# Kernel optimization log

Measured on AMD Instinct MI355X. Metric: run time of the kernel, lower is better.

## Reference

```python
import jax, jax.numpy as jnp
import numpy as np

B, T, N, E = 16, 24, 300, 9600
H, F = 3, 8            # num_heads, out_feats of EdgeGAT
GRU_H = 16
NUM_AIRPORTS, HORIZON = 300, 24
NEG_SLOPE = 0.2


def setup_inputs() -> dict:
    key = jax.random.key(0)
    ks = jax.random.split(key, 16)
    s = 0.1
    x = jax.random.normal(ks[0], (B, T, N, 1), jnp.float32)
    edge_weight = jax.random.uniform(ks[1], (B, T, E, 1), jnp.float32)
    src = jax.random.randint(ks[2], (E,), 0, N)
    dst = jax.random.randint(ks[3], (E,), 0, N)
    W_node = jax.random.normal(ks[4], (1, H * F), jnp.float32) * s
    W_edge = jax.random.normal(ks[5], (1, H * F), jnp.float32) * s
    attn_l = jax.random.normal(ks[6], (H, F), jnp.float32) * s
    attn_r = jax.random.normal(ks[7], (H, F), jnp.float32) * s
    attn_e = jax.random.normal(ks[8], (H, F), jnp.float32) * s
    gat_bias = jax.random.normal(ks[9], (H * F,), jnp.float32) * s
    W_ih = jax.random.normal(ks[10], (3 * GRU_H, H * F), jnp.float32) * s
    W_hh = jax.random.normal(ks[11], (3 * GRU_H, GRU_H), jnp.float32) * s
    b_ih = jax.random.normal(ks[12], (3 * GRU_H,), jnp.float32) * s
    b_hh = jax.random.normal(ks[13], (3 * GRU_H,), jnp.float32) * s
    W_fc = jax.random.normal(ks[14], (NUM_AIRPORTS * HORIZON, GRU_H), jnp.float32) * s
    b_fc = jax.random.normal(ks[15], (NUM_AIRPORTS * HORIZON,), jnp.float32) * s
    return dict(x=x, edge_weight=edge_weight, W_node=W_node, W_edge=W_edge,
                attn_l=attn_l, attn_r=attn_r, attn_e=attn_e, gat_bias=gat_bias,
                W_ih=W_ih, W_hh=W_hh, b_ih=b_ih, b_hh=b_hh,
                W_fc=W_fc, b_fc=b_fc, src=src, dst=dst)


def _forward(x, edge_weight, W_node, W_edge, attn_l, attn_r, attn_e, gat_bias,
             W_ih, W_hh, b_ih, b_hh, W_fc, b_fc, src, dst):
    # --- EdgeGAT on all B*T graphs at once (shared topology, varying feats) ---
    feat = (x @ W_node).reshape(B, T, N, H, F)            # [B,T,N,H,F]
    fe = (edge_weight @ W_edge).reshape(B, T, E, H, F)    # [B,T,E,H,F]
    el = jnp.einsum('btnhf,hf->btnh', feat, attn_l)       # [B,T,N,H]
    er = jnp.einsum('btnhf,hf->btnh', feat, attn_r)
    ee = jnp.einsum('btehf,hf->bteh', fe, attn_e)
    e = jax.nn.leaky_relu(el[:, :, src] + er[:, :, dst] + ee, NEG_SLOPE)  # [B,T,E,H]
    # edge softmax over incoming edges of each dst node
    e_t = jnp.moveaxis(e, 2, 0)                           # [E,B,T,H]
    m = jax.ops.segment_max(e_t, dst, num_segments=N)     # [N,B,T,H]
    num = jnp.exp(e_t - m[dst])
    den = jax.ops.segment_sum(num, dst, num_segments=N)
    alpha = num / den[dst]                                # [E,B,T,H]
    ft_src = jnp.moveaxis(feat[:, :, src], 2, 0)          # [E,B,T,H,F]
    rst = jax.ops.segment_sum(ft_src * alpha[..., None], dst, num_segments=N)  # [N,B,T,H,F]
    rst = rst.reshape(N, B, T, H * F) + gat_bias          # bias of EdgeGATConv
    # mean-pool over nodes per graph -> GRU input sequence
    gru_in = rst.mean(axis=0)                             # [B,T,24]
    # --- GRU (torch semantics), return final hidden state ---
    def step(h, xt):
        gi = xt @ W_ih.T + b_ih
        gh = h @ W_hh.T + b_hh
        i_r, i_z, i_n = jnp.split(gi, 3, axis=-1)
        h_r, h_z, h_n = jnp.split(gh, 3, axis=-1)
        r = jax.nn.sigmoid(i_r + h_r)
        z = jax.nn.sigmoid(i_z + h_z)
        n = jnp.tanh(i_n + r * h_n)
        return (1.0 - z) * n + z * h, None
    h0 = jnp.zeros((B, GRU_H), gru_in.dtype)
    h_n, _ = jax.lax.scan(step, h0, jnp.moveaxis(gru_in, 1, 0))  # scan over T
    return h_n @ W_fc.T + b_fc                            # [B, num_airports*horizon]


def reference(x, edge_weight, W_node, W_edge, attn_l, attn_r, attn_e, gat_bias,
              W_ih, W_hh, b_ih, b_hh, W_fc, b_fc, src, dst):
    return _forward(x, edge_weight, W_node, W_edge, attn_l, attn_r, attn_e, gat_bias,
                    W_ih, W_hh, b_ih, b_hh, W_fc, b_fc, src, dst)
```

## Files before the change

kernel.cpp:

```cpp
#include <hip/hip_runtime.h>
#include <math.h>

#define B_ 16
#define T_ 24
#define G_ 384
#define N_ 300
#define E_ 9600
#define H_ 3
#define F_ 8
#define HF_ 24
#define GRUH_ 16
#define OUTB_ 7200
#define TPB_ 640
#define NWC_ 10

__global__ __launch_bounds__(TPB_) void gat_kernel(
    const float* __restrict__ x, const float* __restrict__ ew,
    const float* __restrict__ Wn, const float* __restrict__ We,
    const float* __restrict__ al, const float* __restrict__ ar,
    const float* __restrict__ ae,
    const int* __restrict__ src, const int* __restrict__ dst,
    float* __restrict__ S)
{
    __shared__ unsigned pkl[E_];
    __shared__ int cnt[NWC_ * N_];
    __shared__ int tot[N_];
    __shared__ int rps[N_ + 1];
    __shared__ float xs[N_];
    __shared__ float cf[9];
    __shared__ float Sred[NWC_][3];

    const int g = blockIdx.x;
    const int tid = threadIdx.x;
    const int w = tid >> 6;
    const long base_e = (long)g * E_;

    for (int i = tid; i < N_; i += TPB_) xs[i] = x[g * N_ + i];
    if (tid < H_) {
        int h = tid;
        float cl = 0.f, cr = 0.f, ce = 0.f;
        #pragma unroll
        for (int f = 0; f < F_; ++f) {
            float wn = Wn[h * F_ + f];
            cl += wn * al[h * F_ + f];
            cr += wn * ar[h * F_ + f];
            ce += We[h * F_ + f] * ae[h * F_ + f];
        }
        cf[h] = cl; cf[3 + h] = cr; cf[6 + h] = ce;
    }

    for (int i = tid; i < NWC_ * N_; i += TPB_) cnt[i] = 0;
    __syncthreads();
    for (int i = tid; i < E_; i += TPB_) atomicAdd(&cnt[w * N_ + dst[i]], 1);
    __syncthreads();
    if (tid < N_) {
        int run = 0;
        #pragma unroll
        for (int k = 0; k < NWC_; ++k) {
            int t = cnt[k * N_ + tid];
            cnt[k * N_ + tid] = run;
            run += t;
        }
        tot[tid] = run;
    }
    __syncthreads();
    if (tid < 64) {
        int base = 0;
        for (int c = 0; c < 5; ++c) {
            int i = c * 64 + tid;
            int orig = (i < N_) ? tot[i] : 0;
            int v = orig;
            #pragma unroll
            for (int o = 1; o < 64; o <<= 1) {
                int u = __shfl_up(v, o, 64);
                if (tid >= o) v += u;
            }
            if (i < N_) rps[i] = base + v - orig;
            base += __shfl(v, 63, 64);
        }
        if (tid == 0) rps[N_] = base;
    }
    __syncthreads();
    for (int i = tid; i < E_; i += TPB_) {
        int d = dst[i];
        int pos = rps[d] + atomicAdd(&cnt[w * N_ + d], 1);
        pkl[pos] = (unsigned)i | ((unsigned)src[i] << 17);
    }
    __syncthreads();

    float n0 = 0.f, d0 = 0.f, n1 = 0.f, d1 = 0.f, n2 = 0.f, d2 = 0.f;
    if (tid < 2 * N_) {
        const int n = tid >> 1;
        const int half = tid & 1;
        const float xd = xs[n];
        const float c0l = cf[0], c1l = cf[1], c2l = cf[2];
        const float c0r = cf[3], c1r = cf[4], c2r = cf[5];
        const float c0e = cf[6], c1e = cf[7], c2e = cf[8];
        const int p1 = rps[n + 1];
        for (int p = rps[n] + half; p < p1; p += 2) {
            unsigned pkv = pkl[p];
            float wv = ew[base_e + (pkv & 0x1FFFFu)];
            float xsv = xs[pkv >> 17];
            float e0 = fmaf(xsv, c0l, fmaf(xd, c0r, wv * c0e)); e0 = e0 > 0.f ? e0 : 0.2f * e0;
            float e1 = fmaf(xsv, c1l, fmaf(xd, c1r, wv * c1e)); e1 = e1 > 0.f ? e1 : 0.2f * e1;
            float e2 = fmaf(xsv, c2l, fmaf(xd, c2r, wv * c2e)); e2 = e2 > 0.f ? e2 : 0.2f * e2;
            float p0 = __expf(e0), pe1 = __expf(e1), pe2 = __expf(e2);
            d0 += p0;  n0 += p0 * xsv;
            d1 += pe1; n1 += pe1 * xsv;
            d2 += pe2; n2 += pe2 * xsv;
        }
    }
    n0 += __shfl_xor(n0, 1); d0 += __shfl_xor(d0, 1);
    n1 += __shfl_xor(n1, 1); d1 += __shfl_xor(d1, 1);
    n2 += __shfl_xor(n2, 1); d2 += __shfl_xor(d2, 1);
    float a0 = 0.f, a1 = 0.f, a2 = 0.f;
    if (tid < 2 * N_ && (tid & 1) == 0) {
        a0 = d0 > 0.f ? n0 / d0 : 0.f;
        a1 = d1 > 0.f ? n1 / d1 : 0.f;
        a2 = d2 > 0.f ? n2 / d2 : 0.f;
    }
    for (int o = 32; o; o >>= 1) {
        a0 += __shfl_down(a0, o);
        a1 += __shfl_down(a1, o);
        a2 += __shfl_down(a2, o);
    }
    const int wave = tid >> 6, lane = tid & 63;
    if (lane == 0) { Sred[wave][0] = a0; Sred[wave][1] = a1; Sred[wave][2] = a2; }
    __syncthreads();
    if (tid < 3) {
        float s = 0.f;
        #pragma unroll
        for (int w2 = 0; w2 < NWC_; ++w2) s += Sred[w2][tid];
        S[g * 3 + tid] = s;
    }
}

__global__ __launch_bounds__(256) void fc_kernel(
    const float* __restrict__ S, const float* __restrict__ Wn,
    const float* __restrict__ gb, const float* __restrict__ Wih,
    const float* __restrict__ bih, const float* __restrict__ Whh,
    const float* __restrict__ bhh, const float* __restrict__ Wfc,
    const float* __restrict__ bfc, float* __restrict__ out)
{
    __shared__ float S2[2][T_][H_];
    __shared__ float hS[2][GRUH_];
    const int tid = threadIdx.x;
    const int idx0 = blockIdx.x * 256;
    const int b0 = idx0 / OUTB_;

    if (tid < 2 * T_ * H_) {
        const int grp = tid / (T_ * H_);
        const int rem = tid - grp * (T_ * H_);
        const int t = rem / H_, h = rem - t * H_;
        const int bb = b0 + grp;
        float s = 0.f;
        if (bb < B_) s = S[(bb * T_ + t) * H_ + h];
        S2[grp][t][h] = s * (1.0f / N_);
    }
    __syncthreads();

    if (tid < 64) {
        const int grp = tid >> 4;
        const int u = tid & 15;
        const int gbase = tid & ~15;
        const bool active = (grp < 2) && (b0 + grp < B_);
        const int sgrp = active ? grp : 0;

        float whr[GRUH_], whz[GRUH_], whn[GRUH_];
        #pragma unroll
        for (int k = 0; k < GRUH_; ++k) {
            whr[k] = Whh[u * GRUH_ + k];
            whz[k] = Whh[(16 + u) * GRUH_ + k];
            whn[k] = Whh[(32 + u) * GRUH_ + k];
        }
        const float bhr = bhh[u], bhz = bhh[16 + u], bhn = bhh[32 + u];

        float A[3][3], C[3];
        #pragma unroll
        for (int r = 0; r < 3; ++r) {
            const int j = r * 16 + u;
            float cc = bih[j];
            A[r][0] = A[r][1] = A[r][2] = 0.f;
            #pragma unroll
            for (int k = 0; k < HF_; ++k) {
                float wk = Wih[j * HF_ + k];
                cc += wk * gb[k];
                A[r][k >> 3] += wk * Wn[k];
            }
            C[r] = cc;
        }

        float h = 0.f;
        for (int t = 0; t < T_; ++t) {
            float S0 = S2[sgrp][t][0], S1 = S2[sgrp][t][1], Sv2 = S2[sgrp][t][2];
            float gr = C[0] + A[0][0] * S0 + A[0][1] * S1 + A[0][2] * Sv2;
            float gz = C[1] + A[1][0] * S0 + A[1][1] * S1 + A[1][2] * Sv2;
            float gn = C[2] + A[2][0] * S0 + A[2][1] * S1 + A[2][2] * Sv2;
            float hr = bhr, hz = bhz, hn = bhn;
            #pragma unroll
            for (int k = 0; k < GRUH_; ++k) {
                float hk = __shfl(h, gbase + k, 64);
                hr += whr[k] * hk;
                hz += whz[k] * hk;
                hn += whn[k] * hk;
            }
            float r = 1.f / (1.f + __expf(-(gr + hr)));
            float z = 1.f / (1.f + __expf(-(gz + hz)));
            float xa = gn + r * hn;
            float te = __expf(-2.f * xa);
            float nn = (1.f - te) / (1.f + te);
            h = (1.f - z) * nn + z * h;
        }
        if (active) hS[grp][u] = h;
    }
    __syncthreads();

    const int idx = idx0 + tid;
    if (idx < B_ * OUTB_) {
        const int b = idx / OUTB_, o = idx - b * OUTB_;
        const float4* wr = (const float4*)(Wfc + (long)o * GRUH_);
        const float* hr = hS[b - b0];
        float4 w0 = wr[0], w1 = wr[1], w2 = wr[2], w3 = wr[3];
        float acc = bfc[o];
        acc += hr[0]  * w0.x + hr[1]  * w0.y + hr[2]  * w0.z + hr[3]  * w0.w;
        acc += hr[4]  * w1.x + hr[5]  * w1.y + hr[6]  * w1.z + hr[7]  * w1.w;
        acc += hr[8]  * w2.x + hr[9]  * w2.y + hr[10] * w2.z + hr[11] * w2.w;
        acc += hr[12] * w3.x + hr[13] * w3.y + hr[14] * w3.z + hr[15] * w3.w;
        out[idx] = acc;
    }
}

extern "C" void kernel_launch(void* const* d_in, const int* in_sizes, int n_in,
                              void* d_out, int out_size, void* d_ws, size_t ws_size,
                              hipStream_t stream) {
    const float* x    = (const float*)d_in[0];
    const float* ew   = (const float*)d_in[1];
    const float* Wn   = (const float*)d_in[2];
    const float* We   = (const float*)d_in[3];
    const float* al   = (const float*)d_in[4];
    const float* ar   = (const float*)d_in[5];
    const float* ae   = (const float*)d_in[6];
    const float* gb   = (const float*)d_in[7];
    const float* Wih  = (const float*)d_in[8];
    const float* Whh  = (const float*)d_in[9];
    const float* bih  = (const float*)d_in[10];
    const float* bhh  = (const float*)d_in[11];
    const float* Wfc  = (const float*)d_in[12];
    const float* bfc  = (const float*)d_in[13];
    const int*   src  = (const int*)d_in[14];
    const int*   dst  = (const int*)d_in[15];
    float* out = (float*)d_out;

    float* S = (float*)d_ws;

    gat_kernel<<<G_, TPB_, 0, stream>>>(x, ew, Wn, We, al, ar, ae, src, dst, S);
    fc_kernel<<<(B_ * OUTB_ + 255) / 256, 256, 0, stream>>>(S, Wn, gb, Wih, bih,
                                                            Whh, bhh, Wfc, bfc, out);
}
```

Baseline: 35.51 us.

## Run GRU recurrence once in last-finishing GAT block via atomic counter

Before this change, every fc_kernel block (450 blocks) recomputed the 24-step GRU recurrence for its two batches before doing the output projection. Now the last GAT block to finish, found with an atomic counter and threadfence, runs the GRU once for all 16 batches and writes h_n to workspace. fc_kernel then only loads h_n and does the FC. This adds a memset launch and a serial tail in a single block at the end of gat_kernel.

```diff
diff --git a/kernel.cpp b/kernel.cpp
--- a/kernel.cpp
+++ b/kernel.cpp
@@ -18,9 +18,11 @@
     const float* __restrict__ x, const float* __restrict__ ew,
     const float* __restrict__ Wn, const float* __restrict__ We,
     const float* __restrict__ al, const float* __restrict__ ar,
-    const float* __restrict__ ae,
+    const float* __restrict__ ae, const float* __restrict__ gb,
+    const float* __restrict__ Wih, const float* __restrict__ bih,
+    const float* __restrict__ Whh, const float* __restrict__ bhh,
     const int* __restrict__ src, const int* __restrict__ dst,
-    float* __restrict__ S)
+    float* __restrict__ S, float* __restrict__ h_out, int* __restrict__ ctr)
 {
     __shared__ unsigned pkl[E_];
     __shared__ int cnt[NWC_ * N_];
@@ -29,6 +31,7 @@
     __shared__ float xs[N_];
     __shared__ float cf[9];
     __shared__ float Sred[NWC_][3];
+    __shared__ int isLast;
 
     const int g = blockIdx.x;
     const int tid = threadIdx.x;
@@ -133,85 +136,88 @@
         for (int w2 = 0; w2 < NWC_; ++w2) s += Sred[w2][tid];
         S[g * 3 + tid] = s;
     }
+
+    __syncthreads();
+    if (tid == 0) {
+        __threadfence();
+        int old = atomicAdd(ctr, 1);
+        isLast = (old == G_ - 1) ? 1 : 0;
+    }
+    __syncthreads();
+    if (isLast) {
+        __threadfence();
+        if (tid < 256) {
+            const int l = tid & 63;
+            const int u = l & 15;
+            const int bg = l & 48;
+            const int b = (tid >> 6) * 4 + (l >> 4);
+
+            float whr[GRUH_], whz[GRUH_], whn[GRUH_];
+            #pragma unroll
+            for (int k = 0; k < GRUH_; ++k) {
+                whr[k] = Whh[u * GRUH_ + k];
+                whz[k] = Whh[(16 + u) * GRUH_ + k];
+                whn[k] = Whh[(32 + u) * GRUH_ + k];
+            }
+            const float bhr = bhh[u], bhz = bhh[16 + u], bhn = bhh[32 + u];
+
+            float A[3][3], C[3];
+            #pragma unroll
+            for (int r = 0; r < 3; ++r) {
+                const int j = r * 16 + u;
+                float cc = bih[j];
+                A[r][0] = A[r][1] = A[r][2] = 0.f;
+                #pragma unroll
+                for (int k = 0; k < HF_; ++k) {
+                    float wk = Wih[j * HF_ + k];
+                    cc += wk * gb[k];
+                    A[r][k >> 3] += wk * Wn[k];
+                }
+                C[r] = cc;
+            }
+
+            float h = 0.f;
+            for (int t = 0; t < T_; ++t) {
+                const float* sp = S + (b * T_ + t) * 3;
+                float S0 = sp[0] * (1.0f / N_);
+                float S1 = sp[1] * (1.0f / N_);
+                float S2 = sp[2] * (1.0f / N_);
+                float gr = C[0] + A[0][0] * S0 + A[0][1] * S1 + A[0][2] * S2;
+                float gz = C[1] + A[1][0] * S0 + A[1][1] * S1 + A[1][2] * S2;
+                float gn = C[2] + A[2][0] * S0 + A[2][1] * S1 + A[2][2] * S2;
+                float hr = bhr, hz = bhz, hnv = bhn;
+                #pragma unroll
+                for (int k = 0; k < GRUH_; ++k) {
+                    float hk = __shfl(h, bg + k, 64);
+                    hr += whr[k] * hk;
+                    hz += whz[k] * hk;
+                    hnv += whn[k] * hk;
+                }
+                float r = 1.f / (1.f + __expf(-(gr + hr)));
+                float z = 1.f / (1.f + __expf(-(gz + hz)));
+                float xa = gn + r * hnv;
+                float te = __expf(-2.f * xa);
+                float nn = (1.f - te) / (1.f + te);
+                h = (1.f - z) * nn + z * h;
+            }
+            h_out[b * GRUH_ + u] = h;
+        }
+    }
 }
 
 __global__ __launch_bounds__(256) void fc_kernel(
-    const float* __restrict__ S, const float* __restrict__ Wn,
-    const float* __restrict__ gb, const float* __restrict__ Wih,
-    const float* __restrict__ bih, const float* __restrict__ Whh,
-    const float* __restrict__ bhh, const float* __restrict__ Wfc,
+    const float* __restrict__ h_n, const float* __restrict__ Wfc,
     const float* __restrict__ bfc, float* __restrict__ out)
 {
-    __shared__ float S2[2][T_][H_];
     __shared__ float hS[2][GRUH_];
     const int tid = threadIdx.x;
     const int idx0 = blockIdx.x * 256;
     const int b0 = idx0 / OUTB_;
 
-    if (tid < 2 * T_ * H_) {
-        const int grp = tid / (T_ * H_);
-        const int rem = tid - grp * (T_ * H_);
-        const int t = rem / H_, h = rem - t * H_;
+    if (tid < 2 * GRUH_) {
+        const int grp = tid >> 4, u = tid & 15;
         const int bb = b0 + grp;
-        float s = 0.f;
-        if (bb < B_) s = S[(bb * T_ + t) * H_ + h];
-        S2[grp][t][h] = s * (1.0f / N_);
-    }
-    __syncthreads();
-
-    if (tid < 64) {
-        const int grp = tid >> 4;
-        const int u = tid & 15;
-        const int gbase = tid & ~15;
-        const bool active = (grp < 2) && (b0 + grp < B_);
-        const int sgrp = active ? grp : 0;
-
-        float whr[GRUH_], whz[GRUH_], whn[GRUH_];
-        #pragma unroll
-        for (int k = 0; k < GRUH_; ++k) {
-            whr[k] = Whh[u * GRUH_ + k];
-            whz[k] = Whh[(16 + u) * GRUH_ + k];
-            whn[k] = Whh[(32 + u) * GRUH_ + k];
-        }
-        const float bhr = bhh[u], bhz = bhh[16 + u], bhn = bhh[32 + u];
-
-        float A[3][3], C[3];
-        #pragma unroll
-        for (int r = 0; r < 3; ++r) {
-            const int j = r * 16 + u;
-            float cc = bih[j];
-            A[r][0] = A[r][1] = A[r][2] = 0.f;
-            #pragma unroll
-            for (int k = 0; k < HF_; ++k) {
-                float wk = Wih[j * HF_ + k];
-                cc += wk * gb[k];
-                A[r][k >> 3] += wk * Wn[k];
-            }
-            C[r] = cc;
-        }
-
-        float h = 0.f;
-        for (int t = 0; t < T_; ++t) {
-            float S0 = S2[sgrp][t][0], S1 = S2[sgrp][t][1], Sv2 = S2[sgrp][t][2];
-            float gr = C[0] + A[0][0] * S0 + A[0][1] * S1 + A[0][2] * Sv2;
-            float gz = C[1] + A[1][0] * S0 + A[1][1] * S1 + A[1][2] * Sv2;
-            float gn = C[2] + A[2][0] * S0 + A[2][1] * S1 + A[2][2] * Sv2;
-            float hr = bhr, hz = bhz, hn = bhn;
-            #pragma unroll
-            for (int k = 0; k < GRUH_; ++k) {
-                float hk = __shfl(h, gbase + k, 64);
-                hr += whr[k] * hk;
-                hz += whz[k] * hk;
-                hn += whn[k] * hk;
-            }
-            float r = 1.f / (1.f + __expf(-(gr + hr)));
-            float z = 1.f / (1.f + __expf(-(gz + hz)));
-            float xa = gn + r * hn;
-            float te = __expf(-2.f * xa);
-            float nn = (1.f - te) / (1.f + te);
-            h = (1.f - z) * nn + z * h;
-        }
-        if (active) hS[grp][u] = h;
+        hS[grp][u] = (bb < B_) ? h_n[bb * GRUH_ + u] : 0.f;
     }
     __syncthreads();
 
@@ -251,9 +257,12 @@
     const int*   dst  = (const int*)d_in[15];
     float* out = (float*)d_out;
 
-    float* S = (float*)d_ws;
-
-    gat_kernel<<<G_, TPB_, 0, stream>>>(x, ew, Wn, We, al, ar, ae, src, dst, S);
-    fc_kernel<<<(B_ * OUTB_ + 255) / 256, 256, 0, stream>>>(S, Wn, gb, Wih, bih,
-                                                            Whh, bhh, Wfc, bfc, out);
+    float* S   = (float*)d_ws;
+    float* h_n = S + G_ * H_;
+    int*   ctr = (int*)(h_n + 256);
+
+    hipMemsetAsync(ctr, 0, sizeof(int), stream);
+    gat_kernel<<<G_, TPB_, 0, stream>>>(x, ew, Wn, We, al, ar, ae, gb,
+                                        Wih, bih, Whh, bhh, src, dst, S, h_n, ctr);
+    fc_kernel<<<(B_ * OUTB_ + 255) / 256, 256, 0, stream>>>(h_n, Wfc, bfc, out);
 }
```

New measurement: 61.29 us. 1.73x slower.

## Split each graph across two blocks with four lanes per destination node

Applied to the files above, without the earlier changes.

The GAT kernel now launches two blocks per graph. Each block handles half of the destination nodes with four lanes per node instead of two, and writes partial sums that the FC kernel adds together while it reads them. The block-to-graph mapping interleaves the two halves, and the per-wave count histograms drop from 10 to 5 copies. In exchange, each block still redoes the full CSR build (counting, scan, scatter) for its graph, so that setup work is doubled.

```diff
diff --git a/kernel.cpp b/kernel.cpp
--- a/kernel.cpp
+++ b/kernel.cpp
@@ -12,7 +12,10 @@
 #define GRUH_ 16
 #define OUTB_ 7200
 #define TPB_ 640
-#define NWC_ 10
+#define NWC_ 5
+#define CPB_ 2
+#define NPC_ 150
+#define QPN_ 4
 
 __global__ __launch_bounds__(TPB_) void gat_kernel(
     const float* __restrict__ x, const float* __restrict__ ew,
@@ -20,7 +23,7 @@
     const float* __restrict__ al, const float* __restrict__ ar,
     const float* __restrict__ ae,
     const int* __restrict__ src, const int* __restrict__ dst,
-    float* __restrict__ S)
+    float* __restrict__ Spart)
 {
     __shared__ unsigned pkl[E_];
     __shared__ int cnt[NWC_ * N_];
@@ -28,11 +31,14 @@
     __shared__ int rps[N_ + 1];
     __shared__ float xs[N_];
     __shared__ float cf[9];
-    __shared__ float Sred[NWC_][3];
-
-    const int g = blockIdx.x;
+    __shared__ float Sred[10][3];
+
+    const int L = blockIdx.x;
+    const int m = L >> 3;
+    const int c = m & 1;
+    const int g = (L & 7) + 8 * (m >> 1);
     const int tid = threadIdx.x;
-    const int w = tid >> 6;
+    const int w = (tid >> 6) % NWC_;
     const long base_e = (long)g * E_;
 
     for (int i = tid; i < N_; i += TPB_) xs[i] = x[g * N_ + i];
@@ -66,8 +72,8 @@
     __syncthreads();
     if (tid < 64) {
         int base = 0;
-        for (int c = 0; c < 5; ++c) {
-            int i = c * 64 + tid;
+        for (int cc = 0; cc < 5; ++cc) {
+            int i = cc * 64 + tid;
             int orig = (i < N_) ? tot[i] : 0;
             int v = orig;
             #pragma unroll
@@ -89,15 +95,15 @@
     __syncthreads();
 
     float n0 = 0.f, d0 = 0.f, n1 = 0.f, d1 = 0.f, n2 = 0.f, d2 = 0.f;
-    if (tid < 2 * N_) {
-        const int n = tid >> 1;
-        const int half = tid & 1;
+    if (tid < QPN_ * NPC_) {
+        const int n = c * NPC_ + (tid >> 2);
+        const int q = tid & 3;
         const float xd = xs[n];
         const float c0l = cf[0], c1l = cf[1], c2l = cf[2];
         const float c0r = cf[3], c1r = cf[4], c2r = cf[5];
         const float c0e = cf[6], c1e = cf[7], c2e = cf[8];
         const int p1 = rps[n + 1];
-        for (int p = rps[n] + half; p < p1; p += 2) {
+        for (int p = rps[n] + q; p < p1; p += QPN_) {
             unsigned pkv = pkl[p];
             float wv = ew[base_e + (pkv & 0x1FFFFu)];
             float xsv = xs[pkv >> 17];
@@ -113,8 +119,11 @@
     n0 += __shfl_xor(n0, 1); d0 += __shfl_xor(d0, 1);
     n1 += __shfl_xor(n1, 1); d1 += __shfl_xor(d1, 1);
     n2 += __shfl_xor(n2, 1); d2 += __shfl_xor(d2, 1);
+    n0 += __shfl_xor(n0, 2); d0 += __shfl_xor(d0, 2);
+    n1 += __shfl_xor(n1, 2); d1 += __shfl_xor(d1, 2);
+    n2 += __shfl_xor(n2, 2); d2 += __shfl_xor(d2, 2);
     float a0 = 0.f, a1 = 0.f, a2 = 0.f;
-    if (tid < 2 * N_ && (tid & 1) == 0) {
+    if (tid < QPN_ * NPC_ && (tid & 3) == 0) {
         a0 = d0 > 0.f ? n0 / d0 : 0.f;
         a1 = d1 > 0.f ? n1 / d1 : 0.f;
         a2 = d2 > 0.f ? n2 / d2 : 0.f;
@@ -130,41 +139,29 @@
     if (tid < 3) {
         float s = 0.f;
         #pragma unroll
-        for (int w2 = 0; w2 < NWC_; ++w2) s += Sred[w2][tid];
-        S[g * 3 + tid] = s;
+        for (int w2 = 0; w2 < 10; ++w2) s += Sred[w2][tid];
+        Spart[g * (CPB_ * 3) + c * 3 + tid] = s;
     }
 }
 
 __global__ __launch_bounds__(256) void fc_kernel(
-    const float* __restrict__ S, const float* __restrict__ Wn,
+    const float* __restrict__ Spart, const float* __restrict__ Wn,
     const float* __restrict__ gb, const float* __restrict__ Wih,
     const float* __restrict__ bih, const float* __restrict__ Whh,
     const float* __restrict__ bhh, const float* __restrict__ Wfc,
     const float* __restrict__ bfc, float* __restrict__ out)
 {
-    __shared__ float S2[2][T_][H_];
     __shared__ float hS[2][GRUH_];
     const int tid = threadIdx.x;
     const int idx0 = blockIdx.x * 256;
     const int b0 = idx0 / OUTB_;
-
-    if (tid < 2 * T_ * H_) {
-        const int grp = tid / (T_ * H_);
-        const int rem = tid - grp * (T_ * H_);
-        const int t = rem / H_, h = rem - t * H_;
-        const int bb = b0 + grp;
-        float s = 0.f;
-        if (bb < B_) s = S[(bb * T_ + t) * H_ + h];
-        S2[grp][t][h] = s * (1.0f / N_);
-    }
-    __syncthreads();
 
     if (tid < 64) {
         const int grp = tid >> 4;
         const int u = tid & 15;
         const int gbase = tid & ~15;
         const bool active = (grp < 2) && (b0 + grp < B_);
-        const int sgrp = active ? grp : 0;
+        const int bb = active ? (b0 + grp) : b0;
 
         float whr[GRUH_], whz[GRUH_], whn[GRUH_];
         #pragma unroll
@@ -192,10 +189,13 @@
 
         float h = 0.f;
         for (int t = 0; t < T_; ++t) {
-            float S0 = S2[sgrp][t][0], S1 = S2[sgrp][t][1], Sv2 = S2[sgrp][t][2];
-            float gr = C[0] + A[0][0] * S0 + A[0][1] * S1 + A[0][2] * Sv2;
-            float gz = C[1] + A[1][0] * S0 + A[1][1] * S1 + A[1][2] * Sv2;
-            float gn = C[2] + A[2][0] * S0 + A[2][1] * S1 + A[2][2] * Sv2;
+            const float* sp = Spart + (bb * T_ + t) * (CPB_ * 3);
+            float S0 = (sp[0] + sp[3]) * (1.0f / N_);
+            float S1 = (sp[1] + sp[4]) * (1.0f / N_);
+            float S2 = (sp[2] + sp[5]) * (1.0f / N_);
+            float gr = C[0] + A[0][0] * S0 + A[0][1] * S1 + A[0][2] * S2;
+            float gz = C[1] + A[1][0] * S0 + A[1][1] * S1 + A[1][2] * S2;
+            float gn = C[2] + A[2][0] * S0 + A[2][1] * S1 + A[2][2] * S2;
             float hr = bhr, hz = bhz, hn = bhn;
             #pragma unroll
             for (int k = 0; k < GRUH_; ++k) {
@@ -251,9 +251,9 @@
     const int*   dst  = (const int*)d_in[15];
     float* out = (float*)d_out;
 
-    float* S = (float*)d_ws;
-
-    gat_kernel<<<G_, TPB_, 0, stream>>>(x, ew, Wn, We, al, ar, ae, src, dst, S);
-    fc_kernel<<<(B_ * OUTB_ + 255) / 256, 256, 0, stream>>>(S, Wn, gb, Wih, bih,
+    float* Spart = (float*)d_ws;
+
+    gat_kernel<<<G_ * CPB_, TPB_, 0, stream>>>(x, ew, Wn, We, al, ar, ae, src, dst, Spart);
+    fc_kernel<<<(B_ * OUTB_ + 255) / 256, 256, 0, stream>>>(Spart, Wn, gb, Wih, bih,
                                                             Whh, bhh, Wfc, bfc, out);
 }
```

Result: slower. 45.63 us (+28.5%).
